# Optimization experiments

Measured on AMD Instinct MI355X. Metric: run time of the kernel, lower is better.

The kernel has to match this reference:

```python
import jax, jax.numpy as jnp
import numpy as np

N = 10000      # atoms
E = 100000     # edges
C = 64         # hidden channels
S = 16         # spherical harmonic components (l_max=3)
NB = 8         # Bessel basis size
HID = 64       # radial MLP hidden
NE = 10        # chemical elements
G = 64         # graphs in batch
L = 2          # interaction layers
HEADS = 1
RC = 5.0       # radial cutoff
AVG_NEI = 16.0


def _sph_l3(u):
    # real spherical harmonics up to l=3, component normalization, on unit vectors u [E,3]
    x, y, z = u[..., 0], u[..., 1], u[..., 2]
    s3 = 3.0 ** 0.5; s5 = 5.0 ** 0.5; s15 = 15.0 ** 0.5
    c1 = (35.0 / 8.0) ** 0.5; c2 = 105.0 ** 0.5; c3 = (21.0 / 8.0) ** 0.5
    c4 = (7.0 / 4.0) ** 0.5; c5 = (105.0 / 4.0) ** 0.5
    comps = [jnp.ones_like(x),
             s3 * x, s3 * y, s3 * z,
             s15 * x * y, s15 * y * z, (s5 / 2) * (3 * z * z - 1), s15 * x * z, (s15 / 2) * (x * x - y * y),
             c1 * y * (3 * x * x - y * y), c2 * x * y * z, c3 * y * (5 * z * z - 1), c4 * z * (5 * z * z - 3),
             c3 * x * (5 * z * z - 1), c5 * z * (x * x - y * y), c1 * x * (x * x - 3 * y * y)]
    return jnp.stack(comps, axis=-1)  # [E, 16]


def _radial(r):
    # Bessel radial basis * polynomial cutoff (p=6); r [E,1] -> [E, NB]
    n = jnp.arange(1, NB + 1, dtype=r.dtype)
    bessel = (2.0 / RC) ** 0.5 * jnp.sin(n * jnp.pi * r / RC) / r
    t = r / RC
    p = 6.0
    fcut = 1.0 - (p + 1) * (p + 2) / 2 * t ** p + p * (p + 2) * t ** (p + 1) - p * (p + 1) / 2 * t ** (p + 2)
    fcut = jnp.where(r < RC, fcut, 0.0)
    return bessel * fcut


def setup_inputs() -> dict:
    key = jax.random.key(0)
    ks = jax.random.split(key, 20)
    positions = jax.random.uniform(ks[0], (N, 3), dtype=jnp.float32) * 6.0
    species = jax.random.randint(ks[1], (N,), 0, NE)
    node_attrs = jax.nn.one_hot(species, NE, dtype=jnp.float32)
    sender = jax.random.randint(ks[2], (E,), 0, N)
    offs = jax.random.randint(ks[3], (E,), 1, N)
    receiver = (sender + offs) % N  # no self loops
    edge_index = jnp.stack([sender, receiver]).astype(jnp.int32)
    batch = jnp.sort(jax.random.randint(ks[4], (N,), 0, G)).astype(jnp.int32)
    head = jnp.zeros((G,), jnp.int32)
    shifts = jnp.zeros((E, 3), jnp.float32)
    ptr = jnp.arange(G + 1, dtype=jnp.int32)
    w = 0.1
    return {
        'positions': positions, 'node_attrs': node_attrs, 'shifts': shifts,
        'atomic_energies': jax.random.normal(ks[5], (HEADS, NE), jnp.float32),
        'W_emb': w * jax.random.normal(ks[6], (NE, C), jnp.float32),
        'W_up': w * jax.random.normal(ks[7], (L, C, C), jnp.float32),
        'mlp_w1': w * jax.random.normal(ks[8], (L, NB, HID), jnp.float32),
        'mlp_w2': w * jax.random.normal(ks[9], (L, HID, HID), jnp.float32),
        'mlp_w3': w * jax.random.normal(ks[10], (L, HID, C * S), jnp.float32),
        'W_mix': w * jax.random.normal(ks[11], (L, C, C), jnp.float32),
        'W_skip': w * jax.random.normal(ks[12], (L, C, NE, C), jnp.float32),
        'Wc': w * jax.random.normal(ks[13], (L, NE, 3, C), jnp.float32),
        'W_out': w * jax.random.normal(ks[14], (L, C, C), jnp.float32),
        'W_ro': w * jax.random.normal(ks[15], (L, C, HEADS), jnp.float32),
        'edge_index': edge_index, 'batch': batch, 'head': head, 'ptr': ptr,
    }


def reference(positions, node_attrs, shifts, atomic_energies, W_emb, W_up, mlp_w1,
              mlp_w2, mlp_w3, W_mix, W_skip, Wc, W_out, W_ro,
              edge_index, batch, head, ptr):
    n_nodes = positions.shape[0]
    n_graphs = ptr.shape[0] - 1
    sender, receiver = edge_index[0], edge_index[1]
    na = jnp.arange(n_nodes)
    node_heads = head[batch]                                   # [N]
    # isolated-atom reference energies
    node_e0 = (node_attrs @ atomic_energies.T)[na, node_heads]  # [N]
    e0 = jax.ops.segment_sum(node_e0, batch, num_segments=n_graphs)
    node_feats = node_attrs @ W_emb                            # [N, C]
    # edge geometry: gather positions by edge index
    vectors = positions[receiver] - positions[sender] + shifts  # [E, 3]
    lengths = jnp.sqrt(jnp.sum(vectors ** 2, axis=-1, keepdims=True))  # [E, 1]
    edge_attrs = _sph_l3(vectors / lengths)                    # [E, S]
    edge_feats = _radial(lengths)                              # [E, NB]
    energies = [e0, jnp.zeros_like(e0)]  # e0, pair_energy (no pair_repulsion)
    for l in range(W_up.shape[0]):
        # radial MLP -> per-edge tensor-product weights
        h = jax.nn.silu(edge_feats @ mlp_w1[l])
        h = jax.nn.silu(h @ mlp_w2[l])
        tp_w = (h @ mlp_w3[l]).reshape(-1, C, S)               # [E, C, S]
        up = node_feats @ W_up[l]                              # [N, C]
        # gather-compute-scatter message passing
        msg = up[sender][:, :, None] * edge_attrs[:, None, :] * tp_w  # [E, C, S]
        A = jax.ops.segment_sum(msg, receiver, num_segments=n_nodes) / AVG_NEI
        A = jnp.einsum('ncs,cd->nds', A, W_mix[l])             # [N, C, S]
        # element-conditioned skip connection
        sc = jnp.einsum('nc,ced,ne->nd', node_feats, W_skip[l], node_attrs)
        # symmetric-contraction product basis (correlation up to 3), element-conditioned
        w = jnp.einsum('ne,ekc->nkc', node_attrs, Wc[l])       # [N, 3, C]
        p1 = A[:, :, 0]
        p2 = jnp.einsum('ncs,ncs->nc', A, A)
        p3 = p2 * p1
        node_feats = (w[:, 0] * p1 + w[:, 1] * p2 + w[:, 2] * p3) @ W_out[l] + sc
        node_en = (node_feats @ W_ro[l])[na, node_heads]       # [N]
        energies.append(jax.ops.segment_sum(node_en, batch, num_segments=n_graphs))
    contributions = jnp.stack(energies, axis=-1)               # [G, L+2]
    return jnp.sum(contributions, axis=-1)                     # [G]
```

## Files before the change

kernel.cpp:

```cpp
#include <hip/hip_runtime.h>

typedef unsigned short u16;
typedef unsigned int u32;
typedef __attribute__((ext_vector_type(8))) short short8;
typedef __attribute__((ext_vector_type(4))) float f32x4;

#define N_NODES 10000
#define N_EDGES 100000
#define C_CH 64
#define S_SPH 16
#define NB_R 8
#define HID_D 64
#define NE_EL 10
#define G_GR 64
#define L_LAY 2
#define N_HEADS 1
#define RCUT 5.0f
#define INV_AVG (1.0f/16.0f)

__device__ __forceinline__ u16 f2bf(float f) {
  u32 u = __float_as_uint(f);
  u32 r = (u + 0x7FFFu + ((u >> 16) & 1u)) >> 16;
  return (u16)r;
}

__global__ void k_init0(float* __restrict__ out, int* __restrict__ deg) {
  int i = blockIdx.x * 256 + threadIdx.x;
  if (i < G_GR) out[i] = 0.0f;
  if (i < N_NODES) deg[i] = 0;
}

__global__ void k_node_init(const float* __restrict__ attrs, const float* __restrict__ ae,
                            const int* __restrict__ batch, const int* __restrict__ head,
                            int* __restrict__ species, float* __restrict__ out) {
  int n = blockIdx.x * 256 + threadIdx.x;
  if (n >= N_NODES) return;
  int sp = 0;
#pragma unroll
  for (int e = 0; e < NE_EL; ++e)
    if (attrs[n * NE_EL + e] > 0.5f) sp = e;
  species[n] = sp;
  int b = batch[n];
  int h = head[b];
  atomicAdd(&out[b], ae[h * NE_EL + sp]);
}

__global__ void k_embed(const int* __restrict__ species, const float* __restrict__ Wemb,
                        float* __restrict__ feats) {
  int idx = blockIdx.x * 256 + threadIdx.x;
  if (idx >= N_NODES * C_CH) return;
  feats[idx] = Wemb[species[idx >> 6] * C_CH + (idx & 63)];
}

__global__ void k_hist(const int* __restrict__ ei, int* __restrict__ deg) {
  int e = blockIdx.x * 256 + threadIdx.x;
  if (e >= N_EDGES) return;
  atomicAdd(&deg[ei[N_EDGES + e]], 1);
}

__global__ void __launch_bounds__(1024) k_scan(const int* __restrict__ deg,
                                               int* __restrict__ rowptr,
                                               int* __restrict__ woff) {
  __shared__ int wsum[16];
  __shared__ int carry_s;
  int tid = threadIdx.x;
  int lane = tid & 63, w = tid >> 6;
  if (tid == 0) carry_s = 0;
  __syncthreads();
  for (int base = 0; base < N_NODES; base += 1024) {
    int i = base + tid;
    int v = (i < N_NODES) ? deg[i] : 0;
    int orig = v;
#pragma unroll
    for (int off = 1; off < 64; off <<= 1) {
      int n = __shfl_up(v, off, 64);
      if (lane >= off) v += n;
    }
    if (lane == 63) wsum[w] = v;
    __syncthreads();
    if (w == 0 && lane < 16) {
      int x = wsum[lane];
#pragma unroll
      for (int off = 1; off < 16; off <<= 1) {
        int n = __shfl_up(x, off, 16);
        if (lane >= off) x += n;
      }
      wsum[lane] = x;
    }
    __syncthreads();
    int waveoff = (w > 0) ? wsum[w - 1] : 0;
    int carry = carry_s;
    int excl = carry + waveoff + v - orig;
    if (i < N_NODES) {
      rowptr[i] = excl;
      woff[i] = excl;
    }
    int tot = wsum[15];
    __syncthreads();
    if (tid == 0) carry_s = carry + tot;
    __syncthreads();
  }
  if (tid == 0) rowptr[N_NODES] = carry_s;
}

__global__ void k_permute(const int* __restrict__ ei, int* __restrict__ woff,
                          int* __restrict__ rank, int* __restrict__ sndp) {
  int e = blockIdx.x * 256 + threadIdx.x;
  if (e >= N_EDGES) return;
  int rdst = ei[N_EDGES + e];
  int pos = atomicAdd(&woff[rdst], 1);
  rank[e] = pos;
  sndp[pos] = ei[e];
}

__global__ void k_geom(const float* __restrict__ pos, const float* __restrict__ shifts,
                       const int* __restrict__ ei, const int* __restrict__ rank,
                       float* __restrict__ Yp, float* __restrict__ radp) {
  int e = blockIdx.x * 256 + threadIdx.x;
  if (e >= N_EDGES) return;
  int s = ei[e], r = ei[N_EDGES + e];
  float dx = pos[r * 3 + 0] - pos[s * 3 + 0] + shifts[e * 3 + 0];
  float dy = pos[r * 3 + 1] - pos[s * 3 + 1] + shifts[e * 3 + 1];
  float dz = pos[r * 3 + 2] - pos[s * 3 + 2] + shifts[e * 3 + 2];
  float rr = sqrtf(dx * dx + dy * dy + dz * dz);
  rr = fmaxf(rr, 1e-12f);
  float inv = 1.0f / rr;
  float x = dx * inv, y = dy * inv, z = dz * inv;
  float xx = x * x, yy = y * y, zz = z * z;
  const float s3 = 1.73205080757f, s5 = 2.2360679775f, s15 = 3.87298334621f;
  const float c1 = 2.09165006634f, c2 = 10.2469507659f, c3 = 1.62018517461f;
  const float c4 = 1.32287565553f, c5 = 5.12347538298f;
  int rk = rank[e];
  float4* Yo = (float4*)(Yp + (size_t)rk * 16);
  Yo[0] = make_float4(1.0f, s3 * x, s3 * y, s3 * z);
  Yo[1] = make_float4(s15 * x * y, s15 * y * z, 0.5f * s5 * (3.0f * zz - 1.0f), s15 * x * z);
  Yo[2] = make_float4(0.5f * s15 * (xx - yy), c1 * y * (3.0f * xx - yy), c2 * x * y * z,
                      c3 * y * (5.0f * zz - 1.0f));
  Yo[3] = make_float4(c4 * z * (5.0f * zz - 3.0f), c3 * x * (5.0f * zz - 1.0f),
                      c5 * z * (xx - yy), c1 * x * (xx - 3.0f * yy));
  float t = rr * (1.0f / RCUT);
  float t2 = t * t;
  float t6 = t2 * t2 * t2;
  float fcut = 1.0f - 28.0f * t6 + 48.0f * t6 * t - 21.0f * t6 * t2;
  if (rr >= RCUT) fcut = 0.0f;
  float pref = 0.63245553203f * inv * fcut;
  float arg = 3.14159265359f * rr * (1.0f / RCUT);
  float sa, ca;
  __sincosf(arg, &sa, &ca);
  float twoc = 2.0f * ca;
  float sprev = 0.0f, scur = sa;
  float rv[8];
#pragma unroll
  for (int n = 0; n < 8; ++n) {
    rv[n] = pref * scur;
    float snext = twoc * scur - sprev;
    sprev = scur;
    scur = snext;
  }
  float4* Ro = (float4*)(radp + (size_t)rk * 8);
  Ro[0] = make_float4(rv[0], rv[1], rv[2], rv[3]);
  Ro[1] = make_float4(rv[4], rv[5], rv[6], rv[7]);
}

__global__ void k_prep(const float* __restrict__ w3, const float* __restrict__ w2,
                       const float* __restrict__ wmix, u16* __restrict__ w3t,
                       u16* __restrict__ w2t, u16* __restrict__ wmixf) {
  int idx = blockIdx.x * 256 + threadIdx.x;
  if (idx < L_LAY * 65536) {
    int l = idx >> 16;
    int r = idx & 65535;
    int k = r & 63;
    int c = (r >> 6) & 63;
    int s = r >> 12;
    w3t[idx] = f2bf(w3[(l * 64 + k) * 1024 + c * 16 + s]);
  } else if (idx < L_LAY * 65536 + L_LAY * 4096) {
    int i = idx - L_LAY * 65536;
    int l = i >> 12;
    int r = i & 4095;
    int t = r >> 6;
    int j = r & 63;
    w2t[l * 4096 + t * 64 + j] = f2bf(w2[(l * 64 + j) * 64 + t]);
  } else if (idx < L_LAY * 65536 + 2 * L_LAY * 4096) {
    int i = idx - L_LAY * 65536 - L_LAY * 4096;
    int l = i >> 12;
    int r = i & 4095;
    int j = r & 7;
    int col = (r >> 3) & 15;
    int kg = (r >> 7) & 3;
    int hf = (r >> 9) & 1;
    int dc = (r >> 10) & 3;
    int c = hf * 32 + kg * 8 + j;
    int d = dc * 16 + col;
    wmixf[l * 4096 + r] = f2bf(wmix[(l * 64 + c) * 64 + d]);
  }
}

__global__ void __launch_bounds__(64) k_edge_mlp(const float* __restrict__ radp,
                                                 const float* __restrict__ w1,
                                                 const u16* __restrict__ w2T,
                                                 u16* __restrict__ h2) {
  __shared__ float w1s[NB_R * HID_D];
  __shared__ __align__(16) u16 h1b[16 * 64];
  int lane = threadIdx.x;
  for (int i = lane; i < NB_R * HID_D; i += 64) w1s[i] = w1[i];
  int er = lane & 15, jg = lane >> 4;
  int eb = blockIdx.x * 16;
  int e = eb + er;
  float4 ra = *(const float4*)(radp + (size_t)e * 8);
  float4 rb = *(const float4*)(radp + (size_t)e * 8 + 4);
  float rv[8] = {ra.x, ra.y, ra.z, ra.w, rb.x, rb.y, rb.z, rb.w};
  u32* hb = (u32*)h1b;
#pragma unroll
  for (int jj = 0; jj < 16; jj += 2) {
    float p0 = 0.f, p1 = 0.f;
#pragma unroll
    for (int k = 0; k < 8; ++k) {
      p0 += rv[k] * w1s[k * 64 + jg * 16 + jj];
      p1 += rv[k] * w1s[k * 64 + jg * 16 + jj + 1];
    }
    p0 = p0 / (1.f + __expf(-p0));
    p1 = p1 / (1.f + __expf(-p1));
    u32 packed = (u32)f2bf(p0) | ((u32)f2bf(p1) << 16);
    int d = jg * 8 + (jj >> 1);
    hb[er * 32 + (d ^ ((er & 7) << 2))] = packed;
  }
  int row = er, kg = jg, col = er;
  const u32* hbr = (const u32*)h1b;
  short8 a0 = *(const short8*)&hbr[row * 32 + ((kg * 4) ^ ((row & 7) << 2))];
  short8 a1 = *(const short8*)&hbr[row * 32 + ((16 + kg * 4) ^ ((row & 7) << 2))];
#pragma unroll
  for (int ch = 0; ch < 4; ++ch) {
    const u16* wp = w2T + (ch * 16 + col) * 64 + kg * 8;
    short8 b0 = *(const short8*)wp;
    short8 b1 = *(const short8*)(wp + 32);
    f32x4 acc = {0.f, 0.f, 0.f, 0.f};
    acc = __builtin_amdgcn_mfma_f32_16x16x32_bf16(a0, b0, acc, 0, 0, 0);
    acc = __builtin_amdgcn_mfma_f32_16x16x32_bf16(a1, b1, acc, 0, 0, 0);
#pragma unroll
    for (int rr = 0; rr < 4; ++rr) {
      float v = acc[rr];
      v = v / (1.f + __expf(-v));
      h2[(size_t)(eb + kg * 4 + rr) * 64 + ch * 16 + col] = f2bf(v);
    }
  }
}

__global__ void __launch_bounds__(256) k_up(const float* __restrict__ feats,
                                            const float* __restrict__ Wup,
                                            float* __restrict__ up) {
  __shared__ float ws[C_CH * C_CH];
  __shared__ float fs[4][C_CH];
  int tid = threadIdx.x;
  for (int i = tid; i < C_CH * C_CH; i += 256) ws[i] = Wup[i];
  __syncthreads();
  int slot = tid >> 6, t = tid & 63;
  for (int nb = blockIdx.x * 4; nb < N_NODES; nb += gridDim.x * 4) {
    int n = nb + slot;
    fs[slot][t] = feats[n * C_CH + t];
    float acc = 0.0f;
#pragma unroll
    for (int j = 0; j < C_CH; ++j) acc += fs[slot][j] * ws[j * C_CH + t];
    up[n * C_CH + t] = acc * INV_AVG;
  }
}

__global__ void __launch_bounds__(256) k_upe(const float* __restrict__ up,
                                             const int* __restrict__ sndp,
                                             float* __restrict__ upe) {
  int tid = threadIdx.x;
  int slot = tid >> 6, t = tid & 63;
  for (int pb = blockIdx.x * 4; pb < N_EDGES; pb += gridDim.x * 4) {
    int pos = pb + slot;
    upe[(size_t)pos * 64 + t] = up[(size_t)sndp[pos] * 64 + t];
  }
}

__global__ void __launch_bounds__(64) k_gather(const u16* __restrict__ h2,
                                               const u16* __restrict__ W3T,
                                               const float* __restrict__ upe,
                                               const float* __restrict__ Yp,
                                               const int* __restrict__ rowptr,
                                               float* __restrict__ Abuf) {
  __shared__ __align__(16) float Yt[16][20];
  int lane = threadIdx.x;
  int row = lane & 15, kg = lane >> 4;
  int col = row;
  int nb = blockIdx.x * 4;
  int rp0 = rowptr[nb], rp1 = rowptr[nb + 1], rp2 = rowptr[nb + 2], rp3 = rowptr[nb + 3],
      rp4 = rowptr[nb + 4];
  int d0 = rp1 - rp0, d1 = rp2 - rp1, d2 = rp3 - rp2, d3 = rp4 - rp3;
  int rmax = max(max((d0 + 3) >> 2, (d1 + 3) >> 2), max((d2 + 3) >> 2, (d3 + 3) >> 2));
  rmax = max(rmax, 1);
  int nr = row >> 2;
  int baseA = nr == 0 ? rp0 : nr == 1 ? rp1 : nr == 2 ? rp2 : rp3;
  int degA = nr == 0 ? d0 : nr == 1 ? d1 : nr == 2 ? d2 : d3;
  int baseR = kg == 0 ? rp0 : kg == 1 ? rp1 : kg == 2 ? rp2 : rp3;
  int degR = kg == 0 ? d0 : kg == 1 ? d1 : kg == 2 ? d2 : d3;
  int nodeR = nb + kg;

#pragma unroll 1
  for (int cg = 0; cg < 4; ++cg) {
#pragma unroll 1
    for (int hf = 0; hf < 2; ++hf) {
      short8 B0[8], B1[8];
#pragma unroll
      for (int ss = 0; ss < 8; ++ss) {
        int s = hf * 8 + ss;
        const u16* wp = W3T + (((s * 64 + cg * 16 + col) << 6) + kg * 8);
        B0[ss] = *(const short8*)wp;
        B1[ss] = *(const short8*)(wp + 32);
      }
      float Areg[8];
#pragma unroll
      for (int ss = 0; ss < 8; ++ss) Areg[ss] = 0.f;
#pragma unroll 1
      for (int r = 0; r < rmax; ++r) {
        int sl = r * 4 + (row & 3);
        short8 a0 = {0, 0, 0, 0, 0, 0, 0, 0};
        short8 a1 = {0, 0, 0, 0, 0, 0, 0, 0};
        float4 yq = make_float4(0.f, 0.f, 0.f, 0.f);
        if (sl < degA) {
          int eA = baseA + sl;
          a0 = *(const short8*)(h2 + (size_t)eA * 64 + kg * 8);
          a1 = *(const short8*)(h2 + (size_t)eA * 64 + 32 + kg * 8);
          yq = *(const float4*)(Yp + (size_t)eA * 16 + kg * 4);
        }
        Yt[kg * 4 + 0][row] = yq.x;
        Yt[kg * 4 + 1][row] = yq.y;
        Yt[kg * 4 + 2][row] = yq.z;
        Yt[kg * 4 + 3][row] = yq.w;
        float upv[4];
#pragma unroll
        for (int q = 0; q < 4; ++q) {
          int slq = r * 4 + q;
          int pos = (slq < degR) ? (baseR + slq) : 0;
          float u = upe[(size_t)pos * 64 + cg * 16 + col];
          upv[q] = (slq < degR) ? u : 0.f;
        }
#pragma unroll
        for (int ss = 0; ss < 8; ++ss) {
          f32x4 acc = {0.f, 0.f, 0.f, 0.f};
          acc = __builtin_amdgcn_mfma_f32_16x16x32_bf16(a0, B0[ss], acc, 0, 0, 0);
          acc = __builtin_amdgcn_mfma_f32_16x16x32_bf16(a1, B1[ss], acc, 0, 0, 0);
          float4 yv = *(const float4*)&Yt[hf * 8 + ss][kg * 4];
          Areg[ss] += acc[0] * yv.x * upv[0] + acc[1] * yv.y * upv[1] + acc[2] * yv.z * upv[2] +
                      acc[3] * yv.w * upv[3];
        }
      }
      float* dst = Abuf + (size_t)nodeR * 1024 + (cg * 16 + col) * 16 + hf * 8;
      *(float4*)(dst + 0) = make_float4(Areg[0], Areg[1], Areg[2], Areg[3]);
      *(float4*)(dst + 4) = make_float4(Areg[4], Areg[5], Areg[6], Areg[7]);
    }
  }
}

__global__ void __launch_bounds__(256) k_node_update(
    const float* __restrict__ Abuf, const float* __restrict__ featsOld,
    float* __restrict__ featsNew, const u16* __restrict__ WmixF,
    const float* __restrict__ Wskip, const float* __restrict__ Wc,
    const float* __restrict__ Wout, const float* __restrict__ Wro,
    const int* __restrict__ species, const int* __restrict__ batch,
    const int* __restrict__ headArr, float* __restrict__ out) {
  __shared__ float Wouts[C_CH * C_CH];
  __shared__ float qs[4][C_CH];
  int tid = threadIdx.x;
  for (int i = tid; i < C_CH * C_CH; i += 256) Wouts[i] = Wout[i];
  int nl = tid >> 6, lane = tid & 63;
  int row = lane & 15, kg = lane >> 4;
  int node = blockIdx.x * 4 + nl;
  int sp = species[node];
  short8 WF[4][2];
#pragma unroll
  for (int dc = 0; dc < 4; ++dc)
#pragma unroll
    for (int hf = 0; hf < 2; ++hf)
      WF[dc][hf] = *(const short8*)(WmixF + (size_t)(dc * 1024 + hf * 512 + kg * 128 + row * 8));
  const float* Arow = Abuf + (size_t)node * 1024;
  short8 a0, a1;
#pragma unroll
  for (int j = 0; j < 8; ++j) {
    a0[j] = (short)f2bf(Arow[(kg * 8 + j) * 16 + row]);
    a1[j] = (short)f2bf(Arow[(32 + kg * 8 + j) * 16 + row]);
  }
#pragma unroll
  for (int dc = 0; dc < 4; ++dc) {
    f32x4 acc = {0.f, 0.f, 0.f, 0.f};
    acc = __builtin_amdgcn_mfma_f32_16x16x32_bf16(a0, WF[dc][0], acc, 0, 0, 0);
    acc = __builtin_amdgcn_mfma_f32_16x16x32_bf16(a1, WF[dc][1], acc, 0, 0, 0);
    float psq = acc[0] * acc[0] + acc[1] * acc[1] + acc[2] * acc[2] + acc[3] * acc[3];
    psq += __shfl_xor(psq, 16, 64);
    psq += __shfl_xor(psq, 32, 64);
    float p1 = __shfl(acc[0], lane & 15, 64);
    float p3 = psq * p1;
    int d = dc * 16 + row;
    float qv = Wc[(sp * 3 + 0) * 64 + d] * p1 + Wc[(sp * 3 + 1) * 64 + d] * psq +
               Wc[(sp * 3 + 2) * 64 + d] * p3;
    if (kg == 0) qs[nl][d] = qv;
  }
  __syncthreads();
  int t = lane;
  const float* frow = featsOld + (size_t)node * 64;
  float sc = 0.0f;
#pragma unroll 8
  for (int c = 0; c < 64; ++c) sc += frow[c] * Wskip[(c * NE_EL + sp) * 64 + t];
  float nf = sc;
#pragma unroll 8
  for (int d = 0; d < 64; ++d) nf += qs[nl][d] * Wouts[d * 64 + t];
  featsNew[(size_t)node * 64 + t] = nf;
  int b = batch[node];
  int h = headArr[b];
  float en = nf * Wro[t * N_HEADS + h];
#pragma unroll
  for (int off = 32; off; off >>= 1) en += __shfl_down(en, off, 64);
  if (t == 0) atomicAdd(&out[b], en);
}

extern "C" void kernel_launch(void* const* d_in, const int* in_sizes, int n_in,
                              void* d_out, int out_size, void* d_ws, size_t ws_size,
                              hipStream_t stream) {
  const float* pos = (const float*)d_in[0];
  const float* attrs = (const float*)d_in[1];
  const float* shifts = (const float*)d_in[2];
  const float* ae = (const float*)d_in[3];
  const float* Wemb = (const float*)d_in[4];
  const float* Wup = (const float*)d_in[5];
  const float* w1 = (const float*)d_in[6];
  const float* w2 = (const float*)d_in[7];
  const float* w3 = (const float*)d_in[8];
  const float* Wmix = (const float*)d_in[9];
  const float* Wskip = (const float*)d_in[10];
  const float* Wc = (const float*)d_in[11];
  const float* Wout = (const float*)d_in[12];
  const float* Wro = (const float*)d_in[13];
  const int* ei = (const int*)d_in[14];
  const int* batch = (const int*)d_in[15];
  const int* head = (const int*)d_in[16];
  float* out = (float*)d_out;

  char* p = (char*)d_ws;
  float* Yp = (float*)p;     p += (size_t)N_EDGES * 16 * 4;
  float* radp = (float*)p;   p += (size_t)N_EDGES * 8 * 4;
  float* up = (float*)p;     p += (size_t)N_NODES * 64 * 4;
  float* upe = (float*)p;    p += (size_t)N_EDGES * 64 * 4;
  float* fA = (float*)p;     p += (size_t)N_NODES * 64 * 4;
  float* fB = (float*)p;     p += (size_t)N_NODES * 64 * 4;
  float* Abuf = (float*)p;   p += (size_t)N_NODES * 1024 * 4;
  u16* h2 = (u16*)p;         p += (size_t)N_EDGES * 64 * 2;
  u16* W3T = (u16*)p;        p += (size_t)L_LAY * 65536 * 2;
  u16* w2T = (u16*)p;        p += (size_t)L_LAY * 4096 * 2;
  u16* WmixF = (u16*)p;      p += (size_t)L_LAY * 4096 * 2;
  int* species = (int*)p;    p += (size_t)N_NODES * 4;
  int* deg = (int*)p;        p += (size_t)N_NODES * 4;
  int* rowptr = (int*)p;     p += (size_t)(N_NODES + 4) * 4;
  int* woff = (int*)p;       p += (size_t)N_NODES * 4;
  int* rank = (int*)p;       p += (size_t)N_EDGES * 4;
  int* sndp = (int*)p;       p += (size_t)N_EDGES * 4;
  if ((size_t)(p - (char*)d_ws) > ws_size) return;

  k_init0<<<(N_NODES + 255) / 256, 256, 0, stream>>>(out, deg);
  k_node_init<<<(N_NODES + 255) / 256, 256, 0, stream>>>(attrs, ae, batch, head, species, out);
  k_embed<<<(N_NODES * C_CH + 255) / 256, 256, 0, stream>>>(species, Wemb, fA);
  k_hist<<<(N_EDGES + 255) / 256, 256, 0, stream>>>(ei, deg);
  k_scan<<<1, 1024, 0, stream>>>(deg, rowptr, woff);
  k_permute<<<(N_EDGES + 255) / 256, 256, 0, stream>>>(ei, woff, rank, sndp);
  k_geom<<<(N_EDGES + 255) / 256, 256, 0, stream>>>(pos, shifts, ei, rank, Yp, radp);
  k_prep<<<(L_LAY * 65536 + 2 * L_LAY * 4096 + 255) / 256, 256, 0, stream>>>(w3, w2, Wmix, W3T,
                                                                             w2T, WmixF);

  const float* fOld = fA;
  float* fNew = fB;
  for (int l = 0; l < L_LAY; ++l) {
    k_edge_mlp<<<N_EDGES / 16, 64, 0, stream>>>(radp, w1 + l * NB_R * HID_D, w2T + l * 4096, h2);
    k_up<<<512, 256, 0, stream>>>(fOld, Wup + l * C_CH * C_CH, up);
    k_upe<<<2048, 256, 0, stream>>>(up, sndp, upe);
    k_gather<<<N_NODES / 4, 64, 0, stream>>>(h2, W3T + l * 65536, upe, Yp, rowptr, Abuf);
    k_node_update<<<N_NODES / 4, 256, 0, stream>>>(
        Abuf, fOld, fNew, WmixF + l * 4096, Wskip + l * C_CH * NE_EL * C_CH,
        Wc + l * NE_EL * 3 * C_CH, Wout + l * C_CH * C_CH, Wro + l * C_CH * N_HEADS,
        species, batch, head, out);
    const float* tmp = fNew;
    fNew = (float*)fOld;
    fOld = tmp;
  }
}
```

Measured before the change: 523.7 us.

## Store aggregated A in bf16 transposed layout and process two nodes per wave

The gather kernel now writes the per-node aggregated tensor A as bf16 in an [s][c] layout instead of fp32 [c][s]. This halves the intermediate buffer traffic, and the node-update kernel can load MFMA operands with vector loads instead of strided scalar loads plus conversion. The node-update kernel also handles two nodes per wavefront, which halves the grid and amortises the Wout shared-memory staging and Wmix fragment loads. The gather store becomes scattered 2-byte writes, which may hurt write coalescing.

```diff
diff --git a/kernel.cpp b/kernel.cpp
--- a/kernel.cpp
+++ b/kernel.cpp
@@ -280,7 +280,7 @@
                                                const float* __restrict__ upe,
                                                const float* __restrict__ Yp,
                                                const int* __restrict__ rowptr,
-                                               float* __restrict__ Abuf) {
+                                               u16* __restrict__ AbufB) {
   __shared__ __align__(16) float Yt[16][20];
   int lane = threadIdx.x;
   int row = lane & 15, kg = lane >> 4;
@@ -347,72 +347,91 @@
                       acc[3] * yv.w * upv[3];
         }
       }
-      float* dst = Abuf + (size_t)nodeR * 1024 + (cg * 16 + col) * 16 + hf * 8;
-      *(float4*)(dst + 0) = make_float4(Areg[0], Areg[1], Areg[2], Areg[3]);
-      *(float4*)(dst + 4) = make_float4(Areg[4], Areg[5], Areg[6], Areg[7]);
+      u16* dst = AbufB + (size_t)nodeR * 1024 + (size_t)(hf * 8) * 64 + (cg * 16 + col);
+#pragma unroll
+      for (int ss = 0; ss < 8; ++ss) dst[ss * 64] = f2bf(Areg[ss]);
     }
   }
 }
 
 __global__ void __launch_bounds__(256) k_node_update(
-    const float* __restrict__ Abuf, const float* __restrict__ featsOld,
+    const u16* __restrict__ AbufB, const float* __restrict__ featsOld,
     float* __restrict__ featsNew, const u16* __restrict__ WmixF,
     const float* __restrict__ Wskip, const float* __restrict__ Wc,
     const float* __restrict__ Wout, const float* __restrict__ Wro,
     const int* __restrict__ species, const int* __restrict__ batch,
     const int* __restrict__ headArr, float* __restrict__ out) {
   __shared__ float Wouts[C_CH * C_CH];
-  __shared__ float qs[4][C_CH];
+  __shared__ float qs[8][C_CH];
   int tid = threadIdx.x;
   for (int i = tid; i < C_CH * C_CH; i += 256) Wouts[i] = Wout[i];
   int nl = tid >> 6, lane = tid & 63;
   int row = lane & 15, kg = lane >> 4;
-  int node = blockIdx.x * 4 + nl;
-  int sp = species[node];
+  int base = blockIdx.x * 8 + nl * 2;
+  int sp0 = species[base], sp1 = species[base + 1];
   short8 WF[4][2];
 #pragma unroll
   for (int dc = 0; dc < 4; ++dc)
 #pragma unroll
     for (int hf = 0; hf < 2; ++hf)
       WF[dc][hf] = *(const short8*)(WmixF + (size_t)(dc * 1024 + hf * 512 + kg * 128 + row * 8));
-  const float* Arow = Abuf + (size_t)node * 1024;
-  short8 a0, a1;
-#pragma unroll
-  for (int j = 0; j < 8; ++j) {
-    a0[j] = (short)f2bf(Arow[(kg * 8 + j) * 16 + row]);
-    a1[j] = (short)f2bf(Arow[(32 + kg * 8 + j) * 16 + row]);
-  }
-#pragma unroll
-  for (int dc = 0; dc < 4; ++dc) {
-    f32x4 acc = {0.f, 0.f, 0.f, 0.f};
-    acc = __builtin_amdgcn_mfma_f32_16x16x32_bf16(a0, WF[dc][0], acc, 0, 0, 0);
-    acc = __builtin_amdgcn_mfma_f32_16x16x32_bf16(a1, WF[dc][1], acc, 0, 0, 0);
-    float psq = acc[0] * acc[0] + acc[1] * acc[1] + acc[2] * acc[2] + acc[3] * acc[3];
-    psq += __shfl_xor(psq, 16, 64);
-    psq += __shfl_xor(psq, 32, 64);
-    float p1 = __shfl(acc[0], lane & 15, 64);
-    float p3 = psq * p1;
-    int d = dc * 16 + row;
-    float qv = Wc[(sp * 3 + 0) * 64 + d] * p1 + Wc[(sp * 3 + 1) * 64 + d] * psq +
-               Wc[(sp * 3 + 2) * 64 + d] * p3;
-    if (kg == 0) qs[nl][d] = qv;
+  const u16* Ar0 = AbufB + (size_t)base * 1024;
+  const u16* Ar1 = Ar0 + 1024;
+  short8 a0n0 = *(const short8*)(Ar0 + row * 64 + kg * 8);
+  short8 a1n0 = *(const short8*)(Ar0 + row * 64 + 32 + kg * 8);
+  short8 a0n1 = *(const short8*)(Ar1 + row * 64 + kg * 8);
+  short8 a1n1 = *(const short8*)(Ar1 + row * 64 + 32 + kg * 8);
+#pragma unroll
+  for (int sub = 0; sub < 2; ++sub) {
+    short8 a0 = sub ? a0n1 : a0n0;
+    short8 a1 = sub ? a1n1 : a1n0;
+    int sp = sub ? sp1 : sp0;
+#pragma unroll
+    for (int dc = 0; dc < 4; ++dc) {
+      f32x4 acc = {0.f, 0.f, 0.f, 0.f};
+      acc = __builtin_amdgcn_mfma_f32_16x16x32_bf16(a0, WF[dc][0], acc, 0, 0, 0);
+      acc = __builtin_amdgcn_mfma_f32_16x16x32_bf16(a1, WF[dc][1], acc, 0, 0, 0);
+      float psq = acc[0] * acc[0] + acc[1] * acc[1] + acc[2] * acc[2] + acc[3] * acc[3];
+      psq += __shfl_xor(psq, 16, 64);
+      psq += __shfl_xor(psq, 32, 64);
+      float p1 = __shfl(acc[0], lane & 15, 64);
+      float p3 = psq * p1;
+      int d = dc * 16 + row;
+      float qv = Wc[(sp * 3 + 0) * 64 + d] * p1 + Wc[(sp * 3 + 1) * 64 + d] * psq +
+                 Wc[(sp * 3 + 2) * 64 + d] * p3;
+      if (kg == 0) qs[nl * 2 + sub][d] = qv;
+    }
   }
   __syncthreads();
   int t = lane;
-  const float* frow = featsOld + (size_t)node * 64;
-  float sc = 0.0f;
+  const float* f0 = featsOld + (size_t)base * 64;
+  const float* f1 = f0 + 64;
+  float sc0 = 0.f, sc1 = 0.f;
 #pragma unroll 8
-  for (int c = 0; c < 64; ++c) sc += frow[c] * Wskip[(c * NE_EL + sp) * 64 + t];
-  float nf = sc;
+  for (int c = 0; c < 64; ++c) {
+    sc0 += f0[c] * Wskip[(c * NE_EL + sp0) * 64 + t];
+    sc1 += f1[c] * Wskip[(c * NE_EL + sp1) * 64 + t];
+  }
+  float nf0 = sc0, nf1 = sc1;
 #pragma unroll 8
-  for (int d = 0; d < 64; ++d) nf += qs[nl][d] * Wouts[d * 64 + t];
-  featsNew[(size_t)node * 64 + t] = nf;
-  int b = batch[node];
-  int h = headArr[b];
-  float en = nf * Wro[t * N_HEADS + h];
-#pragma unroll
-  for (int off = 32; off; off >>= 1) en += __shfl_down(en, off, 64);
-  if (t == 0) atomicAdd(&out[b], en);
+  for (int d = 0; d < 64; ++d) {
+    nf0 += qs[nl * 2 + 0][d] * Wouts[d * 64 + t];
+    nf1 += qs[nl * 2 + 1][d] * Wouts[d * 64 + t];
+  }
+  featsNew[(size_t)base * 64 + t] = nf0;
+  featsNew[(size_t)(base + 1) * 64 + t] = nf1;
+  int b0 = batch[base], b1 = batch[base + 1];
+  float en0 = nf0 * Wro[t * N_HEADS + headArr[b0]];
+  float en1 = nf1 * Wro[t * N_HEADS + headArr[b1]];
+#pragma unroll
+  for (int off = 32; off; off >>= 1) {
+    en0 += __shfl_down(en0, off, 64);
+    en1 += __shfl_down(en1, off, 64);
+  }
+  if (t == 0) {
+    atomicAdd(&out[b0], en0);
+    atomicAdd(&out[b1], en1);
+  }
 }
 
 extern "C" void kernel_launch(void* const* d_in, const int* in_sizes, int n_in,
@@ -444,7 +463,7 @@
   float* upe = (float*)p;    p += (size_t)N_EDGES * 64 * 4;
   float* fA = (float*)p;     p += (size_t)N_NODES * 64 * 4;
   float* fB = (float*)p;     p += (size_t)N_NODES * 64 * 4;
-  float* Abuf = (float*)p;   p += (size_t)N_NODES * 1024 * 4;
+  u16* AbufB = (u16*)p;      p += (size_t)N_NODES * 1024 * 2;
   u16* h2 = (u16*)p;         p += (size_t)N_EDGES * 64 * 2;
   u16* W3T = (u16*)p;        p += (size_t)L_LAY * 65536 * 2;
   u16* w2T = (u16*)p;        p += (size_t)L_LAY * 4096 * 2;
@@ -473,9 +492,9 @@
     k_edge_mlp<<<N_EDGES / 16, 64, 0, stream>>>(radp, w1 + l * NB_R * HID_D, w2T + l * 4096, h2);
     k_up<<<512, 256, 0, stream>>>(fOld, Wup + l * C_CH * C_CH, up);
     k_upe<<<2048, 256, 0, stream>>>(up, sndp, upe);
-    k_gather<<<N_NODES / 4, 64, 0, stream>>>(h2, W3T + l * 65536, upe, Yp, rowptr, Abuf);
-    k_node_update<<<N_NODES / 4, 256, 0, stream>>>(
-        Abuf, fOld, fNew, WmixF + l * 4096, Wskip + l * C_CH * NE_EL * C_CH,
+    k_gather<<<N_NODES / 4, 64, 0, stream>>>(h2, W3T + l * 65536, upe, Yp, rowptr, AbufB);
+    k_node_update<<<N_NODES / 8, 256, 0, stream>>>(
+        AbufB, fOld, fNew, WmixF + l * 4096, Wskip + l * C_CH * NE_EL * C_CH,
         Wc + l * NE_EL * 3 * C_CH, Wout + l * C_CH * C_CH, Wro + l * C_CH * N_HEADS,
         species, batch, head, out);
     const float* tmp = fNew;
```

After: 505.1 us. 3.6% less time.

## Fuse node update into gather kernel, keeping A tile in LDS as bf16

Applied to the files above, without the earlier changes.

Merges the node-update step into the gather kernel. Each 64-thread block now writes its four nodes' aggregated A tensors to shared memory as bf16 and runs the mix MFMA, symmetric contraction, skip, output projection and energy readout itself. This removes the round trip of the large fp32 Abuf through global memory and one kernel launch per layer. In exchange, the node-update work runs on one wavefront that loops serially over four nodes, and Wout is read from global memory instead of being staged in shared memory, which may lengthen the gather kernel.

```diff
diff --git a/kernel.cpp b/kernel.cpp
--- a/kernel.cpp
+++ b/kernel.cpp
@@ -275,17 +275,25 @@
   }
 }
 
-__global__ void __launch_bounds__(64) k_gather(const u16* __restrict__ h2,
-                                               const u16* __restrict__ W3T,
-                                               const float* __restrict__ upe,
-                                               const float* __restrict__ Yp,
-                                               const int* __restrict__ rowptr,
-                                               float* __restrict__ Abuf) {
+__global__ void __launch_bounds__(64) k_gather_fused(
+    const u16* __restrict__ h2, const u16* __restrict__ W3T, const float* __restrict__ upe,
+    const float* __restrict__ Yp, const int* __restrict__ rowptr,
+    const u16* __restrict__ WmixF, const float* __restrict__ featsOld,
+    float* __restrict__ featsNew, const float* __restrict__ Wskip,
+    const float* __restrict__ Wc, const float* __restrict__ WoutG,
+    const float* __restrict__ Wro, const int* __restrict__ species,
+    const int* __restrict__ batch, const int* __restrict__ headArr,
+    float* __restrict__ out) {
   __shared__ __align__(16) float Yt[16][20];
+  __shared__ __align__(16) u16 Asub[4][16][72];
+  __shared__ float qs[4][64];
+  __shared__ float fsub[4][64];
   int lane = threadIdx.x;
   int row = lane & 15, kg = lane >> 4;
   int col = row;
   int nb = blockIdx.x * 4;
+#pragma unroll
+  for (int k = 0; k < 4; ++k) fsub[k][lane] = featsOld[(size_t)(nb + k) * 64 + lane];
   int rp0 = rowptr[nb], rp1 = rowptr[nb + 1], rp2 = rowptr[nb + 2], rp3 = rowptr[nb + 3],
       rp4 = rowptr[nb + 4];
   int d0 = rp1 - rp0, d1 = rp2 - rp1, d2 = rp3 - rp2, d3 = rp4 - rp3;
@@ -296,7 +304,6 @@
   int degA = nr == 0 ? d0 : nr == 1 ? d1 : nr == 2 ? d2 : d3;
   int baseR = kg == 0 ? rp0 : kg == 1 ? rp1 : kg == 2 ? rp2 : rp3;
   int degR = kg == 0 ? d0 : kg == 1 ? d1 : kg == 2 ? d2 : d3;
-  int nodeR = nb + kg;
 
 #pragma unroll 1
   for (int cg = 0; cg < 4; ++cg) {
@@ -347,72 +354,70 @@
                       acc[3] * yv.w * upv[3];
         }
       }
-      float* dst = Abuf + (size_t)nodeR * 1024 + (cg * 16 + col) * 16 + hf * 8;
-      *(float4*)(dst + 0) = make_float4(Areg[0], Areg[1], Areg[2], Areg[3]);
-      *(float4*)(dst + 4) = make_float4(Areg[4], Areg[5], Areg[6], Areg[7]);
-    }
-  }
-}
-
-__global__ void __launch_bounds__(256) k_node_update(
-    const float* __restrict__ Abuf, const float* __restrict__ featsOld,
-    float* __restrict__ featsNew, const u16* __restrict__ WmixF,
-    const float* __restrict__ Wskip, const float* __restrict__ Wc,
-    const float* __restrict__ Wout, const float* __restrict__ Wro,
-    const int* __restrict__ species, const int* __restrict__ batch,
-    const int* __restrict__ headArr, float* __restrict__ out) {
-  __shared__ float Wouts[C_CH * C_CH];
-  __shared__ float qs[4][C_CH];
-  int tid = threadIdx.x;
-  for (int i = tid; i < C_CH * C_CH; i += 256) Wouts[i] = Wout[i];
-  int nl = tid >> 6, lane = tid & 63;
-  int row = lane & 15, kg = lane >> 4;
-  int node = blockIdx.x * 4 + nl;
-  int sp = species[node];
+#pragma unroll
+      for (int ss = 0; ss < 8; ++ss) Asub[kg][hf * 8 + ss][cg * 16 + col] = f2bf(Areg[ss]);
+    }
+  }
+  __syncthreads();
+
   short8 WF[4][2];
 #pragma unroll
   for (int dc = 0; dc < 4; ++dc)
 #pragma unroll
     for (int hf = 0; hf < 2; ++hf)
       WF[dc][hf] = *(const short8*)(WmixF + (size_t)(dc * 1024 + hf * 512 + kg * 128 + row * 8));
-  const float* Arow = Abuf + (size_t)node * 1024;
-  short8 a0, a1;
-#pragma unroll
-  for (int j = 0; j < 8; ++j) {
-    a0[j] = (short)f2bf(Arow[(kg * 8 + j) * 16 + row]);
-    a1[j] = (short)f2bf(Arow[(32 + kg * 8 + j) * 16 + row]);
-  }
-#pragma unroll
-  for (int dc = 0; dc < 4; ++dc) {
-    f32x4 acc = {0.f, 0.f, 0.f, 0.f};
-    acc = __builtin_amdgcn_mfma_f32_16x16x32_bf16(a0, WF[dc][0], acc, 0, 0, 0);
-    acc = __builtin_amdgcn_mfma_f32_16x16x32_bf16(a1, WF[dc][1], acc, 0, 0, 0);
-    float psq = acc[0] * acc[0] + acc[1] * acc[1] + acc[2] * acc[2] + acc[3] * acc[3];
-    psq += __shfl_xor(psq, 16, 64);
-    psq += __shfl_xor(psq, 32, 64);
-    float p1 = __shfl(acc[0], lane & 15, 64);
-    float p3 = psq * p1;
-    int d = dc * 16 + row;
-    float qv = Wc[(sp * 3 + 0) * 64 + d] * p1 + Wc[(sp * 3 + 1) * 64 + d] * psq +
-               Wc[(sp * 3 + 2) * 64 + d] * p3;
-    if (kg == 0) qs[nl][d] = qv;
+  int spArr[4];
+#pragma unroll
+  for (int k = 0; k < 4; ++k) spArr[k] = species[nb + k];
+#pragma unroll 1
+  for (int i = 0; i < 4; ++i) {
+    short8 a0 = *(const short8*)&Asub[i][row][kg * 8];
+    short8 a1 = *(const short8*)&Asub[i][row][32 + kg * 8];
+    int sp = spArr[i];
+#pragma unroll
+    for (int dc = 0; dc < 4; ++dc) {
+      f32x4 acc = {0.f, 0.f, 0.f, 0.f};
+      acc = __builtin_amdgcn_mfma_f32_16x16x32_bf16(a0, WF[dc][0], acc, 0, 0, 0);
+      acc = __builtin_amdgcn_mfma_f32_16x16x32_bf16(a1, WF[dc][1], acc, 0, 0, 0);
+      float psq = acc[0] * acc[0] + acc[1] * acc[1] + acc[2] * acc[2] + acc[3] * acc[3];
+      psq += __shfl_xor(psq, 16, 64);
+      psq += __shfl_xor(psq, 32, 64);
+      float p1 = __shfl(acc[0], lane & 15, 64);
+      float p3 = psq * p1;
+      int d = dc * 16 + row;
+      float qv = Wc[(sp * 3 + 0) * 64 + d] * p1 + Wc[(sp * 3 + 1) * 64 + d] * psq +
+                 Wc[(sp * 3 + 2) * 64 + d] * p3;
+      if (kg == 0) qs[i][d] = qv;
+    }
   }
   __syncthreads();
+
   int t = lane;
-  const float* frow = featsOld + (size_t)node * 64;
-  float sc = 0.0f;
+  float en[4];
+  int bArr[4];
+#pragma unroll 1
+  for (int i = 0; i < 4; ++i) {
+    int sp = spArr[i];
+    float sc = 0.f;
 #pragma unroll 8
-  for (int c = 0; c < 64; ++c) sc += frow[c] * Wskip[(c * NE_EL + sp) * 64 + t];
-  float nf = sc;
+    for (int c = 0; c < 64; ++c) sc += fsub[i][c] * Wskip[(c * NE_EL + sp) * 64 + t];
+    float v = sc;
 #pragma unroll 8
-  for (int d = 0; d < 64; ++d) nf += qs[nl][d] * Wouts[d * 64 + t];
-  featsNew[(size_t)node * 64 + t] = nf;
-  int b = batch[node];
-  int h = headArr[b];
-  float en = nf * Wro[t * N_HEADS + h];
-#pragma unroll
-  for (int off = 32; off; off >>= 1) en += __shfl_down(en, off, 64);
-  if (t == 0) atomicAdd(&out[b], en);
+    for (int d = 0; d < 64; ++d) v += qs[i][d] * WoutG[d * 64 + t];
+    featsNew[(size_t)(nb + i) * 64 + t] = v;
+    int b = batch[nb + i];
+    bArr[i] = b;
+    en[i] = v * Wro[t * N_HEADS + headArr[b]];
+  }
+#pragma unroll
+  for (int off = 32; off; off >>= 1) {
+#pragma unroll
+    for (int i = 0; i < 4; ++i) en[i] += __shfl_down(en[i], off, 64);
+  }
+  if (lane == 0) {
+#pragma unroll
+    for (int i = 0; i < 4; ++i) atomicAdd(&out[bArr[i]], en[i]);
+  }
 }
 
 extern "C" void kernel_launch(void* const* d_in, const int* in_sizes, int n_in,
@@ -444,7 +449,6 @@
   float* upe = (float*)p;    p += (size_t)N_EDGES * 64 * 4;
   float* fA = (float*)p;     p += (size_t)N_NODES * 64 * 4;
   float* fB = (float*)p;     p += (size_t)N_NODES * 64 * 4;
-  float* Abuf = (float*)p;   p += (size_t)N_NODES * 1024 * 4;
   u16* h2 = (u16*)p;         p += (size_t)N_EDGES * 64 * 2;
   u16* W3T = (u16*)p;        p += (size_t)L_LAY * 65536 * 2;
   u16* w2T = (u16*)p;        p += (size_t)L_LAY * 4096 * 2;
@@ -473,11 +477,10 @@
     k_edge_mlp<<<N_EDGES / 16, 64, 0, stream>>>(radp, w1 + l * NB_R * HID_D, w2T + l * 4096, h2);
     k_up<<<512, 256, 0, stream>>>(fOld, Wup + l * C_CH * C_CH, up);
     k_upe<<<2048, 256, 0, stream>>>(up, sndp, upe);
-    k_gather<<<N_NODES / 4, 64, 0, stream>>>(h2, W3T + l * 65536, upe, Yp, rowptr, Abuf);
-    k_node_update<<<N_NODES / 4, 256, 0, stream>>>(
-        Abuf, fOld, fNew, WmixF + l * 4096, Wskip + l * C_CH * NE_EL * C_CH,
-        Wc + l * NE_EL * 3 * C_CH, Wout + l * C_CH * C_CH, Wro + l * C_CH * N_HEADS,
-        species, batch, head, out);
+    k_gather_fused<<<N_NODES / 4, 64, 0, stream>>>(
+        h2, W3T + l * 65536, upe, Yp, rowptr, WmixF + l * 4096, fOld, fNew,
+        Wskip + l * C_CH * NE_EL * C_CH, Wc + l * NE_EL * 3 * C_CH, Wout + l * C_CH * C_CH,
+        Wro + l * C_CH * N_HEADS, species, batch, head, out);
     const float* tmp = fNew;
     fNew = (float*)fOld;
     fOld = tmp;
```

Result: faster. 450.5 us (-14.0%).
